# Optimization experiments

Hardware: AMD Instinct MI355X
Metric: run time of the kernel (lower is better)

The kernel has to match this reference:

```python
import jax, jax.numpy as jnp
import numpy as np

NUM_HEADS = 12


def setup_inputs() -> dict:
    key = jax.random.key(0)
    k1, k2, k3 = jax.random.split(key, 3)
    B, N, C = 8, 1024, 768
    x = jax.random.normal(k1, (B, N, C), dtype=jnp.float32)
    qkv_w = jax.random.normal(k2, (3 * C, C), dtype=jnp.float32) * (C ** -0.5)
    proj_w = jax.random.normal(k3, (C, C), dtype=jnp.float32) * (C ** -0.5)
    proj_b = jnp.zeros((C,), dtype=jnp.float32)
    return {"x": x, "qkv_w": qkv_w, "proj_w": proj_w, "proj_b": proj_b, "cur_depth": 9}


def reference(x, qkv_w, proj_w, proj_b, cur_depth):
    B, N, C = x.shape
    H = NUM_HEADS
    hd = C // H
    scale = hd ** -0.5
    # qkv projection (no bias): (B,N,3C) -> (3,B,H,N,hd)
    qkv = (x @ qkv_w.T).reshape(B, N, 3, H, hd).transpose(2, 0, 3, 1, 4)
    q, k, v = qkv[0], qkv[1], qkv[2]
    # full attention scores, materialized as in the original
    attn = jnp.einsum("bhqd,bhkd->bhqk", q, k) * scale  # (B,H,N,N)
    # sigmoid gate from the LAST query row's pre-softmax scores, averaged over heads
    # attn[:, :, -1, :] -> (B,H,N); mean over heads -> (B,N); broadcast to (B,1,1,N)
    mask = jax.nn.sigmoid(attn[:, :, -1, :].mean(axis=1))[:, None, None, :]
    attn = jax.nn.softmax(attn, axis=-1)
    if cur_depth >= 9:
        attn = attn * mask
    out = jnp.einsum("bhqk,bhkd->bhqd", attn, v)  # (B,H,N,hd)
    out = out.transpose(0, 2, 1, 3).reshape(B, N, C)
    out = out @ proj_w.T + proj_b
    return (out, mask)
```

## Files before the change

kernel.cpp:

```cpp
#include <hip/hip_runtime.h>
#include <stdint.h>

typedef __bf16 bf16;
typedef __bf16 bf16x8 __attribute__((ext_vector_type(8)));
typedef float f32x4 __attribute__((ext_vector_type(4)));
typedef float f32x16 __attribute__((ext_vector_type(16)));
typedef uint32_t u32x4 __attribute__((ext_vector_type(4)));

#define DEVI static __device__ __forceinline__

DEVI void async_ld16(void* lds, const void* g) {
  __builtin_amdgcn_global_load_lds(
      (const __attribute__((address_space(1))) void*)(uintptr_t)g,
      (__attribute__((address_space(3))) void*)(uint32_t)(uintptr_t)lds,
      16, 0, 0);
}

DEVI f32x4 vsplat(float v) { f32x4 r; r.x = v; r.y = v; r.z = v; r.w = v; return r; }

__global__ __launch_bounds__(256) void cvt3_kernel(
    const float* __restrict__ x, bf16* __restrict__ xb,
    const float* __restrict__ w1, bf16* __restrict__ w1b,
    const float* __restrict__ w2, bf16* __restrict__ w2b) {
  int i = blockIdx.x * 256 + threadIdx.x;
  const float* src; bf16* dst; int idx;
  if (i < 786432) { src = x; dst = xb; idx = i; }
  else if (i < 786432 + 221184) { src = w1; dst = w1b; idx = i - 786432; }
  else if (i < 786432 + 221184 + 73728) { src = w2; dst = w2b; idx = i - 1007616; }
  else return;
  const float4* p = (const float4*)src + (size_t)idx * 2;
  float4 a = p[0], b = p[1];
  bf16x8 o;
  o[0] = (bf16)a.x; o[1] = (bf16)a.y; o[2] = (bf16)a.z; o[3] = (bf16)a.w;
  o[4] = (bf16)b.x; o[5] = (bf16)b.y; o[6] = (bf16)b.z; o[7] = (bf16)b.w;
  *((bf16x8*)dst + idx) = o;
}

template <int MODE>
__global__ __launch_bounds__(256) void gemm_bt_kernel(
    const bf16* __restrict__ A, const bf16* __restrict__ B, int K, int N,
    bf16* __restrict__ q_out, bf16* __restrict__ k_out, bf16* __restrict__ vt_out,
    float* __restrict__ f_out, const float* __restrict__ bias) {
  __shared__ bf16 As[128 * 32];
  __shared__ bf16 Bs[128 * 32];
  const int t = threadIdx.x;
  const int lane = t & 63, g = lane >> 4, ql = lane & 15;
  const int w = t >> 6, wr = w >> 1, wc = w & 1;
  const int wbase = __builtin_amdgcn_readfirstlane(t & 192);
  const int m0 = blockIdx.y * 128, n0 = blockIdx.x * 128;

  f32x4 acc[4][4];
#pragma unroll
  for (int i = 0; i < 4; i++)
#pragma unroll
    for (int j = 0; j < 4; j++) acc[i][j] = vsplat(0.f);

  for (int kt = 0; kt < K; kt += 32) {
    __syncthreads();
#pragma unroll
    for (int i = 0; i < 2; i++) {
      int unit = i * 256 + t;
      int row = unit >> 2;
      int su = (unit & 3) ^ ((row >> 1) & 3);
      async_ld16(As + (size_t)(i * 256 + wbase) * 8,
                 A + (size_t)(m0 + row) * K + kt + su * 8);
      async_ld16(Bs + (size_t)(i * 256 + wbase) * 8,
                 B + (size_t)(n0 + row) * K + kt + su * 8);
    }
    __syncthreads();
    bf16x8 af[4], bfr[4];
#pragma unroll
    for (int f = 0; f < 4; f++) {
      int ra = wr * 64 + f * 16 + ql;
      af[f] = *(const bf16x8*)(As + ra * 32 + ((g ^ ((ra >> 1) & 3)) * 8));
      int rb = wc * 64 + f * 16 + ql;
      bfr[f] = *(const bf16x8*)(Bs + rb * 32 + ((g ^ ((rb >> 1) & 3)) * 8));
    }
#pragma unroll
    for (int fm = 0; fm < 4; fm++)
#pragma unroll
      for (int fn = 0; fn < 4; fn++)
        acc[fm][fn] = __builtin_amdgcn_mfma_f32_16x16x32_bf16(af[fm], bfr[fn],
                                                              acc[fm][fn], 0, 0, 0);
  }

  if (MODE == 0) {
#pragma unroll
    for (int fm = 0; fm < 4; fm++) {
#pragma unroll
      for (int fn = 0; fn < 4; fn++) {
        int n = n0 + wc * 64 + fn * 16 + ql;
#pragma unroll
        for (int r = 0; r < 4; r++) {
          int m = m0 + wr * 64 + fm * 16 + g * 4 + r;
          int b = m >> 10, nn = m & 1023;
          float v = acc[fm][fn][r];
          if (n < 768) {
            int h = n >> 6, d = n & 63;
            q_out[((size_t)((b * 12 + h) * 1024 + nn)) * 64 + d] = (bf16)(v * 0.125f);
          } else if (n < 1536) {
            int c = n - 768, h = c >> 6, d = c & 63;
            k_out[((size_t)((b * 12 + h) * 1024 + nn)) * 64 + d] = (bf16)v;
          } else {
            int c = n - 1536, h = c >> 6, d = c & 63;
            vt_out[((size_t)((b * 12 + h) * 64 + d)) * 1024 + nn] = (bf16)v;
          }
        }
      }
    }
  } else {
#pragma unroll
    for (int fm = 0; fm < 4; fm++) {
#pragma unroll
      for (int fn = 0; fn < 4; fn++) {
        int n = n0 + wc * 64 + fn * 16 + ql;
        float bv = bias[n];
#pragma unroll
        for (int r = 0; r < 4; r++) {
          int m = m0 + wr * 64 + fm * 16 + g * 4 + r;
          f_out[(size_t)m * N + n] = acc[fm][fn][r] + bv;
        }
      }
    }
  }
}

__global__ __launch_bounds__(256) void mask_kernel(
    const bf16* __restrict__ qb, const bf16* __restrict__ kb, float* __restrict__ mout) {
  int t = threadIdx.x, lane = t & 63;
  int wid = blockIdx.x * 4 + (t >> 6);
  int b = wid >> 10, kcol = wid & 1023;
  float acc = 0.f;
#pragma unroll
  for (int h = 0; h < 12; h++) {
    const bf16* qr = qb + ((size_t)((b * 12 + h) * 1024 + 1023)) * 64;
    const bf16* kr = kb + ((size_t)((b * 12 + h) * 1024 + kcol)) * 64;
    acc += (float)qr[lane] * (float)kr[lane];
  }
#pragma unroll
  for (int off = 32; off >= 1; off >>= 1) acc += __shfl_xor(acc, off);
  if (lane == 0) {
    float x = acc * (1.f / 12.f);
    mout[(b << 10) + kcol] = 1.f / (1.f + __expf(-x));
  }
}

__global__ __launch_bounds__(256) void vscale_kernel(
    bf16* __restrict__ vt, const float* __restrict__ maskp, const int* __restrict__ cdp) {
  const bool am = (cdp[0] >= 9);
  int i = blockIdx.x * 256 + threadIdx.x;
  int row = i >> 7, gcol = i & 127;
  size_t off = ((size_t)blockIdx.y * 768 + row) * 1024 + gcol * 8;
  const float* mp = maskp + blockIdx.y * 1024 + gcol * 8;
  float4 m0 = *(const float4*)mp;
  float4 m1 = *(const float4*)(mp + 4);
  float mm[8] = {m0.x, m0.y, m0.z, m0.w, m1.x, m1.y, m1.z, m1.w};
  bf16x8 v = *(bf16x8*)(vt + off);
#pragma unroll
  for (int e = 0; e < 8; e++) {
    float f = am ? mm[e] : 1.0f;
    v[e] = (bf16)((float)v[e] * f);
  }
  *(bf16x8*)(vt + off) = v;
}

__global__ __launch_bounds__(256) void attn_kernel(
    const bf16* __restrict__ qb, const bf16* __restrict__ kb,
    const bf16* __restrict__ vt, bf16* __restrict__ ob) {
  __shared__ bf16 Ks[64 * 64];
  __shared__ bf16 Vs[64 * 64];
  const int t = threadIdx.x;
  const int lane = t & 63, j = lane & 31, hi = lane >> 5;
  const int w = t >> 6;
  const int wbase = __builtin_amdgcn_readfirstlane(t & 192);
  int bid = (blockIdx.x & 7) * 96 + (blockIdx.x >> 3);
  const int bh = bid >> 3, qt = bid & 7;
  const int b = bh / 12, h = bh - b * 12;
  const bf16* Qp = qb + (size_t)bh * 65536;
  const bf16* Kp = kb + (size_t)bh * 65536;
  const bf16* Vp = vt + (size_t)bh * 65536;
  const int q0 = qt * 128 + w * 32;

  bf16x8 qf[4];
#pragma unroll
  for (int ds = 0; ds < 4; ds++)
    qf[ds] = *(const bf16x8*)(Qp + (size_t)(q0 + j) * 64 + hi * 8 + ds * 16);

  f32x16 o0, o1;
#pragma unroll
  for (int i = 0; i < 16; i++) { o0[i] = 0.f; o1[i] = 0.f; }
  float m = -1e30f, D = 0.f;

  for (int kv0 = 0; kv0 < 1024; kv0 += 64) {
    __syncthreads();
#pragma unroll
    for (int i = 0; i < 2; i++) {
      int unit = i * 256 + t;
      int row = unit >> 3;
      int su = (unit & 7) ^ (row & 7);
      async_ld16(Ks + (size_t)(i * 256 + wbase) * 8,
                 Kp + (size_t)(kv0 + row) * 64 + su * 8);
      async_ld16(Vs + (size_t)(i * 256 + wbase) * 8,
                 Vp + (size_t)row * 1024 + kv0 + su * 8);
    }
    __syncthreads();

    f32x16 s0, s1;
#pragma unroll
    for (int i = 0; i < 16; i++) { s0[i] = 0.f; s1[i] = 0.f; }
#pragma unroll
    for (int ds = 0; ds < 4; ds++) {
      int c = hi + 2 * ds;
      bf16x8 k0 = *(const bf16x8*)(Ks + j * 64 + ((c ^ (j & 7)) * 8));
      s0 = __builtin_amdgcn_mfma_f32_32x32x16_bf16(k0, qf[ds], s0, 0, 0, 0);
      int r1 = 32 + j;
      bf16x8 k1 = *(const bf16x8*)(Ks + r1 * 64 + ((c ^ (r1 & 7)) * 8));
      s1 = __builtin_amdgcn_mfma_f32_32x32x16_bf16(k1, qf[ds], s1, 0, 0, 0);
    }

    float tm = s0[0];
#pragma unroll
    for (int i = 1; i < 16; i++) tm = fmaxf(tm, s0[i]);
#pragma unroll
    for (int i = 0; i < 16; i++) tm = fmaxf(tm, s1[i]);
    tm = fmaxf(tm, __shfl_xor(tm, 32));
    if (!__all(tm <= m + 8.f)) {
      float mn = fmaxf(m, tm);
      float sc = __expf(m - mn);
      m = mn;
      D *= sc;
#pragma unroll
      for (int i = 0; i < 16; i++) { o0[i] *= sc; o1[i] *= sc; }
    }
#pragma unroll
    for (int i = 0; i < 16; i++) s0[i] = __expf(s0[i] - m);
#pragma unroll
    for (int i = 0; i < 16; i++) s1[i] = __expf(s1[i] - m);
    float rs = 0.f;
#pragma unroll
    for (int i = 0; i < 16; i++) rs += s0[i] + s1[i];
    rs += __shfl_xor(rs, 32);
    D += rs;

    bf16x8 pf[4];
#pragma unroll
    for (int ks = 0; ks < 4; ks++) {
      int base = 8 * (ks & 1);
      float pA0, pA1, pB0, pB1, pA2, pA3, pB2, pB3;
      if (ks & 2) {
        pA0 = s1[base]; pA1 = s1[base + 1]; pB0 = s1[base + 4]; pB1 = s1[base + 5];
        pA2 = s1[base + 2]; pA3 = s1[base + 3]; pB2 = s1[base + 6]; pB3 = s1[base + 7];
      } else {
        pA0 = s0[base]; pA1 = s0[base + 1]; pB0 = s0[base + 4]; pB1 = s0[base + 5];
        pA2 = s0[base + 2]; pA3 = s0[base + 3]; pB2 = s0[base + 6]; pB3 = s0[base + 7];
      }
      uint32_t CA, CB, CA2, CB2;
      asm("v_cvt_pk_bf16_f32 %0, %1, %2" : "=v"(CA) : "v"(pA0), "v"(pA1));
      asm("v_cvt_pk_bf16_f32 %0, %1, %2" : "=v"(CB) : "v"(pB0), "v"(pB1));
      asm("v_permlane32_swap_b32 %0, %1" : "+v"(CA), "+v"(CB));
      asm("v_cvt_pk_bf16_f32 %0, %1, %2" : "=v"(CA2) : "v"(pA2), "v"(pA3));
      asm("v_cvt_pk_bf16_f32 %0, %1, %2" : "=v"(CB2) : "v"(pB2), "v"(pB3));
      asm("v_permlane32_swap_b32 %0, %1" : "+v"(CA2), "+v"(CB2));
      u32x4 dw;
      dw[0] = CA; dw[1] = CA2; dw[2] = CB; dw[3] = CB2;
      pf[ks] = __builtin_bit_cast(bf16x8, dw);
    }

#pragma unroll
    for (int ks = 0; ks < 4; ks++) {
      int c = hi + 2 * ks;
      bf16x8 v0 = *(const bf16x8*)(Vs + j * 64 + ((c ^ (j & 7)) * 8));
      o0 = __builtin_amdgcn_mfma_f32_32x32x16_bf16(pf[ks], v0, o0, 0, 0, 0);
      int r1 = 32 + j;
      bf16x8 v1 = *(const bf16x8*)(Vs + r1 * 64 + ((c ^ (r1 & 7)) * 8));
      o1 = __builtin_amdgcn_mfma_f32_32x32x16_bf16(pf[ks], v1, o1, 0, 0, 0);
    }
  }

  float dinv = 1.f / D;
#pragma unroll
  for (int reg = 0; reg < 16; reg++) {
    int qrow = (reg & 3) + 8 * (reg >> 2) + 4 * hi;
    float dv = __shfl(dinv, qrow);
    bf16* dst = ob + (size_t)(b * 1024 + q0 + qrow) * 768 + h * 64 + j;
    dst[0]  = (bf16)(o0[reg] * dv);
    dst[32] = (bf16)(o1[reg] * dv);
  }
}

extern "C" void kernel_launch(void* const* d_in, const int* in_sizes, int n_in,
                              void* d_out, int out_size, void* d_ws, size_t ws_size,
                              hipStream_t stream) {
  const float* x     = (const float*)d_in[0];
  const float* qkvw  = (const float*)d_in[1];
  const float* projw = (const float*)d_in[2];
  const float* projb = (const float*)d_in[3];
  const int*   cd    = (const int*)d_in[4];
  float* out  = (float*)d_out;
  float* mout = out + 6291456;

  char* p = (char*)d_ws;
  bf16* xb    = (bf16*)p; p += 12582912;
  bf16* wqkvb = (bf16*)p; p += 3538944;
  bf16* wpb   = (bf16*)p; p += 1179648;
  bf16* qb    = (bf16*)p; p += 12582912;
  bf16* kb    = (bf16*)p; p += 12582912;
  bf16* vtb   = (bf16*)p; p += 12582912;
  bf16* obuf  = xb;

  cvt3_kernel<<<4224, 256, 0, stream>>>(x, xb, qkvw, wqkvb, projw, wpb);
  gemm_bt_kernel<0><<<dim3(18, 64), 256, 0, stream>>>(
      xb, wqkvb, 768, 2304, qb, kb, vtb, nullptr, nullptr);
  mask_kernel<<<2048, 256, 0, stream>>>(qb, kb, mout);
  vscale_kernel<<<dim3(384, 8), 256, 0, stream>>>(vtb, mout, cd);
  attn_kernel<<<768, 256, 0, stream>>>(qb, kb, vtb, obuf);
  gemm_bt_kernel<1><<<dim3(6, 64), 256, 0, stream>>>(
      obuf, wpb, 768, 768, nullptr, nullptr, nullptr, out, projb);
}
```

Baseline: 239.8 us.

## Double-buffer LDS tiles in GEMM and attention, remap GEMM blocks per XCD

Both the GEMM and the attention kernel now use two LDS buffers. The next K/V or A/B tile is issued asynchronously before computing on the current one, and one barrier per iteration replaces two. The goal is to overlap global-to-LDS traffic with MFMA work, at the cost of doubled shared memory, which may reduce occupancy. GEMM launches become 1D, with a block index remapped so that each XCD handles contiguous row tiles for L2 locality. s_setprio is raised around the MFMA sections.

```diff
diff --git a/kernel.cpp b/kernel.cpp
--- a/kernel.cpp
+++ b/kernel.cpp
@@ -36,18 +36,36 @@
   *((bf16x8*)dst + idx) = o;
 }
 
+DEVI void gemm_stage(bf16* AsD, bf16* BsD, const bf16* A, const bf16* B,
+                     int K, int m0, int n0, int kt, int t, int wbase) {
+#pragma unroll
+  for (int i = 0; i < 2; i++) {
+    int unit = i * 256 + t;
+    int row = unit >> 2;
+    int su = (unit & 3) ^ ((row >> 1) & 3);
+    async_ld16(AsD + (size_t)(i * 256 + wbase) * 8,
+               A + (size_t)(m0 + row) * K + kt + su * 8);
+    async_ld16(BsD + (size_t)(i * 256 + wbase) * 8,
+               B + (size_t)(n0 + row) * K + kt + su * 8);
+  }
+}
+
 template <int MODE>
 __global__ __launch_bounds__(256) void gemm_bt_kernel(
     const bf16* __restrict__ A, const bf16* __restrict__ B, int K, int N,
-    bf16* __restrict__ q_out, bf16* __restrict__ k_out, bf16* __restrict__ vt_out,
-    float* __restrict__ f_out, const float* __restrict__ bias) {
-  __shared__ bf16 As[128 * 32];
-  __shared__ bf16 Bs[128 * 32];
+    int nx, bf16* __restrict__ q_out, bf16* __restrict__ k_out,
+    bf16* __restrict__ vt_out, float* __restrict__ f_out,
+    const float* __restrict__ bias) {
+  __shared__ bf16 As[2][128 * 32];
+  __shared__ bf16 Bs[2][128 * 32];
   const int t = threadIdx.x;
   const int lane = t & 63, g = lane >> 4, ql = lane & 15;
   const int w = t >> 6, wr = w >> 1, wc = w & 1;
   const int wbase = __builtin_amdgcn_readfirstlane(t & 192);
-  const int m0 = blockIdx.y * 128, n0 = blockIdx.x * 128;
+  const int bid = blockIdx.x;
+  const int xcd = bid & 7, i6 = bid >> 3;
+  const int yq = i6 / nx;
+  const int m0 = (xcd * 8 + yq) * 128, n0 = (i6 - yq * nx) * 128;
 
   f32x4 acc[4][4];
 #pragma unroll
@@ -55,33 +73,31 @@
 #pragma unroll
     for (int j = 0; j < 4; j++) acc[i][j] = vsplat(0.f);
 
+  gemm_stage(As[0], Bs[0], A, B, K, m0, n0, 0, t, wbase);
+  int cur = 0;
   for (int kt = 0; kt < K; kt += 32) {
     __syncthreads();
-#pragma unroll
-    for (int i = 0; i < 2; i++) {
-      int unit = i * 256 + t;
-      int row = unit >> 2;
-      int su = (unit & 3) ^ ((row >> 1) & 3);
-      async_ld16(As + (size_t)(i * 256 + wbase) * 8,
-                 A + (size_t)(m0 + row) * K + kt + su * 8);
-      async_ld16(Bs + (size_t)(i * 256 + wbase) * 8,
-                 B + (size_t)(n0 + row) * K + kt + su * 8);
-    }
-    __syncthreads();
+    if (kt + 32 < K)
+      gemm_stage(As[cur ^ 1], Bs[cur ^ 1], A, B, K, m0, n0, kt + 32, t, wbase);
+    const bf16* Asc = As[cur];
+    const bf16* Bsc = Bs[cur];
     bf16x8 af[4], bfr[4];
 #pragma unroll
     for (int f = 0; f < 4; f++) {
       int ra = wr * 64 + f * 16 + ql;
-      af[f] = *(const bf16x8*)(As + ra * 32 + ((g ^ ((ra >> 1) & 3)) * 8));
+      af[f] = *(const bf16x8*)(Asc + ra * 32 + ((g ^ ((ra >> 1) & 3)) * 8));
       int rb = wc * 64 + f * 16 + ql;
-      bfr[f] = *(const bf16x8*)(Bs + rb * 32 + ((g ^ ((rb >> 1) & 3)) * 8));
-    }
+      bfr[f] = *(const bf16x8*)(Bsc + rb * 32 + ((g ^ ((rb >> 1) & 3)) * 8));
+    }
+    __builtin_amdgcn_s_setprio(1);
 #pragma unroll
     for (int fm = 0; fm < 4; fm++)
 #pragma unroll
       for (int fn = 0; fn < 4; fn++)
         acc[fm][fn] = __builtin_amdgcn_mfma_f32_16x16x32_bf16(af[fm], bfr[fn],
                                                               acc[fm][fn], 0, 0, 0);
+    __builtin_amdgcn_s_setprio(0);
+    cur ^= 1;
   }
 
   if (MODE == 0) {
@@ -164,11 +180,25 @@
   *(bf16x8*)(vt + off) = v;
 }
 
+DEVI void attn_stage(bf16* KsD, bf16* VsD, const bf16* Kp, const bf16* Vp,
+                     int kv0, int t, int wbase) {
+#pragma unroll
+  for (int i = 0; i < 2; i++) {
+    int unit = i * 256 + t;
+    int row = unit >> 3;
+    int su = (unit & 7) ^ (row & 7);
+    async_ld16(KsD + (size_t)(i * 256 + wbase) * 8,
+               Kp + (size_t)(kv0 + row) * 64 + su * 8);
+    async_ld16(VsD + (size_t)(i * 256 + wbase) * 8,
+               Vp + (size_t)row * 1024 + kv0 + su * 8);
+  }
+}
+
 __global__ __launch_bounds__(256) void attn_kernel(
     const bf16* __restrict__ qb, const bf16* __restrict__ kb,
     const bf16* __restrict__ vt, bf16* __restrict__ ob) {
-  __shared__ bf16 Ks[64 * 64];
-  __shared__ bf16 Vs[64 * 64];
+  __shared__ bf16 Ks[2][64 * 64];
+  __shared__ bf16 Vs[2][64 * 64];
   const int t = threadIdx.x;
   const int lane = t & 63, j = lane & 31, hi = lane >> 5;
   const int w = t >> 6;
@@ -191,32 +221,29 @@
   for (int i = 0; i < 16; i++) { o0[i] = 0.f; o1[i] = 0.f; }
   float m = -1e30f, D = 0.f;
 
+  attn_stage(Ks[0], Vs[0], Kp, Vp, 0, t, wbase);
+  int cur = 0;
   for (int kv0 = 0; kv0 < 1024; kv0 += 64) {
     __syncthreads();
-#pragma unroll
-    for (int i = 0; i < 2; i++) {
-      int unit = i * 256 + t;
-      int row = unit >> 3;
-      int su = (unit & 7) ^ (row & 7);
-      async_ld16(Ks + (size_t)(i * 256 + wbase) * 8,
-                 Kp + (size_t)(kv0 + row) * 64 + su * 8);
-      async_ld16(Vs + (size_t)(i * 256 + wbase) * 8,
-                 Vp + (size_t)row * 1024 + kv0 + su * 8);
-    }
-    __syncthreads();
+    if (kv0 + 64 < 1024)
+      attn_stage(Ks[cur ^ 1], Vs[cur ^ 1], Kp, Vp, kv0 + 64, t, wbase);
+    const bf16* Ksc = Ks[cur];
+    const bf16* Vsc = Vs[cur];
 
     f32x16 s0, s1;
 #pragma unroll
     for (int i = 0; i < 16; i++) { s0[i] = 0.f; s1[i] = 0.f; }
+    __builtin_amdgcn_s_setprio(1);
 #pragma unroll
     for (int ds = 0; ds < 4; ds++) {
       int c = hi + 2 * ds;
-      bf16x8 k0 = *(const bf16x8*)(Ks + j * 64 + ((c ^ (j & 7)) * 8));
+      bf16x8 k0 = *(const bf16x8*)(Ksc + j * 64 + ((c ^ (j & 7)) * 8));
       s0 = __builtin_amdgcn_mfma_f32_32x32x16_bf16(k0, qf[ds], s0, 0, 0, 0);
       int r1 = 32 + j;
-      bf16x8 k1 = *(const bf16x8*)(Ks + r1 * 64 + ((c ^ (r1 & 7)) * 8));
+      bf16x8 k1 = *(const bf16x8*)(Ksc + r1 * 64 + ((c ^ (r1 & 7)) * 8));
       s1 = __builtin_amdgcn_mfma_f32_32x32x16_bf16(k1, qf[ds], s1, 0, 0, 0);
     }
+    __builtin_amdgcn_s_setprio(0);
 
     float tm = s0[0];
 #pragma unroll
@@ -266,15 +293,18 @@
       pf[ks] = __builtin_bit_cast(bf16x8, dw);
     }
 
+    __builtin_amdgcn_s_setprio(1);
 #pragma unroll
     for (int ks = 0; ks < 4; ks++) {
       int c = hi + 2 * ks;
-      bf16x8 v0 = *(const bf16x8*)(Vs + j * 64 + ((c ^ (j & 7)) * 8));
+      bf16x8 v0 = *(const bf16x8*)(Vsc + j * 64 + ((c ^ (j & 7)) * 8));
       o0 = __builtin_amdgcn_mfma_f32_32x32x16_bf16(pf[ks], v0, o0, 0, 0, 0);
       int r1 = 32 + j;
-      bf16x8 v1 = *(const bf16x8*)(Vs + r1 * 64 + ((c ^ (r1 & 7)) * 8));
+      bf16x8 v1 = *(const bf16x8*)(Vsc + r1 * 64 + ((c ^ (r1 & 7)) * 8));
       o1 = __builtin_amdgcn_mfma_f32_32x32x16_bf16(pf[ks], v1, o1, 0, 0, 0);
     }
+    __builtin_amdgcn_s_setprio(0);
+    cur ^= 1;
   }
 
   float dinv = 1.f / D;
@@ -309,11 +339,11 @@
   bf16* obuf  = xb;
 
   cvt3_kernel<<<4224, 256, 0, stream>>>(x, xb, qkvw, wqkvb, projw, wpb);
-  gemm_bt_kernel<0><<<dim3(18, 64), 256, 0, stream>>>(
-      xb, wqkvb, 768, 2304, qb, kb, vtb, nullptr, nullptr);
+  gemm_bt_kernel<0><<<1152, 256, 0, stream>>>(
+      xb, wqkvb, 768, 2304, 18, qb, kb, vtb, nullptr, nullptr);
   mask_kernel<<<2048, 256, 0, stream>>>(qb, kb, mout);
   vscale_kernel<<<dim3(384, 8), 256, 0, stream>>>(vtb, mout, cd);
   attn_kernel<<<768, 256, 0, stream>>>(qb, kb, vtb, obuf);
-  gemm_bt_kernel<1><<<dim3(6, 64), 256, 0, stream>>>(
-      obuf, wpb, 768, 768, nullptr, nullptr, nullptr, out, projb);
-}
+  gemm_bt_kernel<1><<<384, 256, 0, stream>>>(
+      obuf, wpb, 768, 768, 6, nullptr, nullptr, nullptr, out, projb);
+}
```

After: 216.0 us. 10.0% less time.
